# Kernel tuning notes

Hardware: AMD Instinct MI355X
Metric: run time of the kernel (lower is better)

Reference implementation:

```python
import jax, jax.numpy as jnp
import numpy as np

ND, NC = 100000, 20000
E_DD, E_DC, E_CD = 1600000, 800000, 800000
DDIM, CDIM, H, B = 256, 512, 128, 100000


def _lin_init(k, out_d, in_d):
    kw, kb = jax.random.split(k)
    s = 1.0 / np.sqrt(in_d)
    return (jax.random.uniform(kw, (out_d, in_d), jnp.float32, -s, s),
            jax.random.uniform(kb, (out_d,), jnp.float32, -s, s))


def setup_inputs() -> dict:
    key = jax.random.key(0)
    ks = jax.random.split(key, 32)
    inp = {
        'x_drug': jax.random.normal(ks[0], (ND, DDIM), jnp.float32),
        'x_cell': jax.random.normal(ks[1], (NC, CDIM), jnp.float32),
        'ei_dd_src': jax.random.randint(ks[2], (E_DD,), 0, ND),
        'ei_dd_dst': jax.random.randint(ks[3], (E_DD,), 0, ND),
        'ei_dc_src': jax.random.randint(ks[4], (E_DC,), 0, ND),
        'ei_dc_dst': jax.random.randint(ks[5], (E_DC,), 0, NC),
        'ei_cd_src': jax.random.randint(ks[6], (E_CD,), 0, NC),
        'ei_cd_dst': jax.random.randint(ks[7], (E_CD,), 0, ND),
        'q_da': jax.random.randint(ks[8], (B,), 0, ND),
        'q_db': jax.random.randint(ks[9], (B,), 0, ND),
        'q_c': jax.random.randint(ks[10], (B,), 0, NC),
    }
    # input projections
    inp['wd'], inp['bd'] = _lin_init(ks[11], H, DDIM)
    inp['wc'], inp['bc'] = _lin_init(ks[12], H, CDIM)
    # per-edge-type SAGEConv params: lin_l (W+b, on aggregated neighbors), lin_r (W only, on root)
    i = 13
    for name in ['dd1', 'cd1', 'dc1', 'dd2', 'cd2', 'dc2']:
        wl, bl = _lin_init(ks[i], H, H)
        wr, _ = _lin_init(ks[i + 1], H, H)
        inp[name + '_wl'], inp[name + '_bl'], inp[name + '_wr'] = wl, bl, wr
        i += 2
    # MLP head
    inp['m1_w'], inp['m1_b'] = _lin_init(ks[i], H, 3 * H)
    inp['m2_w'], inp['m2_b'] = _lin_init(ks[i + 1], 1, H)
    return inp


def _sage(x_src, x_dst, src, dst, wl, bl, wr):
    # SAGEConv: mean-aggregate neighbor (src) features onto dst, then lin_l + lin_r(root)
    n_dst = x_dst.shape[0]
    agg = jax.ops.segment_sum(x_src[src], dst, num_segments=n_dst)  # [n_dst, H]
    cnt = jax.ops.segment_sum(jnp.ones(src.shape, x_src.dtype), dst, num_segments=n_dst)
    mean = agg / jnp.maximum(cnt, 1.0)[:, None]
    return mean @ wl.T + bl + x_dst @ wr.T


def reference(x_drug, x_cell, wd, bd, wc, bc,
              dd1_wl, dd1_bl, dd1_wr, cd1_wl, cd1_bl, cd1_wr, dc1_wl, dc1_bl, dc1_wr,
              dd2_wl, dd2_bl, dd2_wr, cd2_wl, cd2_bl, cd2_wr, dc2_wl, dc2_bl, dc2_wr,
              m1_w, m1_b, m2_w, m2_b,
              ei_dd_src, ei_dd_dst, ei_dc_src, ei_dc_dst, ei_cd_src, ei_cd_dst,
              q_da, q_db, q_c):
    xd = x_drug @ wd.T + bd  # [ND, H]
    xc = x_cell @ wc.T + bc  # [NC, H]
    # layer 1 (to_hetero: sum contributions per dst node type, then relu)
    hd = jax.nn.relu(_sage(xd, xd, ei_dd_src, ei_dd_dst, dd1_wl, dd1_bl, dd1_wr)
                     + _sage(xc, xd, ei_cd_src, ei_cd_dst, cd1_wl, cd1_bl, cd1_wr))
    hc = jax.nn.relu(_sage(xd, xc, ei_dc_src, ei_dc_dst, dc1_wl, dc1_bl, dc1_wr))
    # layer 2 (no activation)
    od = (_sage(hd, hd, ei_dd_src, ei_dd_dst, dd2_wl, dd2_bl, dd2_wr)
          + _sage(hc, hd, ei_cd_src, ei_cd_dst, cd2_wl, cd2_bl, cd2_wr))
    oc = _sage(hd, hc, ei_dc_src, ei_dc_dst, dc2_wl, dc2_bl, dc2_wr)
    combined = jnp.concatenate([od[q_da], od[q_db], oc[q_c]], axis=-1)  # [B, 3H]
    h = jax.nn.relu(combined @ m1_w.T + m1_b)  # dropout is eval-mode identity
    return (h @ m2_w.T + m2_b)[:, 0]
```

## Files before the change

### kernel.cpp

```cpp
#include <hip/hip_runtime.h>
#include <hip/hip_fp16.h>

typedef _Float16 f16;
typedef f16 f16x8 __attribute__((ext_vector_type(8)));
typedef float f32x4 __attribute__((ext_vector_type(4)));

#define NDRUG 100000
#define NCELL 20000
#define EDD   1600000
#define EDC   800000
#define ECD   800000
#define NQ    100000
#define ETOT  (EDD + ECD + EDC)
#define NNODE 220000

#define NBD 782
#define NBC 313
#define NBTOT (NBD + NBC)
#define ECHUNK 8192
#define NBLK ((ETOT + ECHUNK - 1) / ECHUNK)
#define BCAP 8192
#define LCAP 6144

__device__ inline int bucket_of(int rdst) { return rdst < 200000 ? (rdst >> 8) : NBD + ((rdst - 200000) >> 6); }
__device__ inline int dl_of(int rdst)     { return rdst < 200000 ? (rdst & 255) : ((rdst - 200000) & 63); }


__global__ void initcur_k(int* __restrict__ cur)
{
    int i = blockIdx.x * 256 + threadIdx.x;
    if (i < NBTOT) cur[i] = i * BCAP;
}


__global__ __launch_bounds__(256) void scatter_k(
    const int* __restrict__ dds, const int* __restrict__ ddd,
    const int* __restrict__ cds, const int* __restrict__ cdd,
    const int* __restrict__ dcs, const int* __restrict__ dcd,
    int* __restrict__ bucket_cur, unsigned* __restrict__ binned)
{
    __shared__ int lh[NBTOT];
    __shared__ int lbase[NBTOT];

    int tid = threadIdx.x;
    for (int i = tid; i < NBTOT; i += 256) lh[i] = 0;
    __syncthreads();

    int base = blockIdx.x * ECHUNK;
    int end = base + ECHUNK; if (end > ETOT) end = ETOT;

    for (int e = base + tid; e < end; e += 256) {
        int rdst;
        if (e < EDD) rdst = ddd[e];
        else if (e < EDD + ECD) rdst = 100000 + cdd[e - EDD];
        else rdst = 200000 + dcd[e - EDD - ECD];
        atomicAdd(&lh[bucket_of(rdst)], 1);
    }
    __syncthreads();

    for (int i = tid; i < NBTOT; i += 256) {
        int c = lh[i];
        lbase[i] = c ? atomicAdd(&bucket_cur[i], c) : 0;
        lh[i] = 0;
    }
    __syncthreads();

    for (int e = base + tid; e < end; e += 256) {
        int src, rdst;
        if (e < EDD) { src = dds[e]; rdst = ddd[e]; }
        else if (e < EDD + ECD) { int i2 = e - EDD; src = cds[i2]; rdst = 100000 + cdd[i2]; }
        else { int i2 = e - EDD - ECD; src = dcs[i2]; rdst = 200000 + dcd[i2]; }
        int b = bucket_of(rdst);
        int r = atomicAdd(&lh[b], 1);
        binned[lbase[b] + r] = ((unsigned)dl_of(rdst) << 17) | (unsigned)src;
    }
}


__global__ __launch_bounds__(256) void scan_pbase_k(const int* __restrict__ bucket_cur,
                                                    int* __restrict__ pbase, int* __restrict__ rowptr)
{
    __shared__ int seg[256];
    int tid = threadIdx.x;
    int mine[5], s = 0;
#pragma unroll
    for (int q = 0; q < 5; ++q) {
        int idx = tid * 5 + q;
        int t = 0;
        if (idx < NBTOT) {
            t = bucket_cur[idx] - idx * BCAP;
            t = t < 0 ? 0 : (t > LCAP ? LCAP : t);
        }
        mine[q] = t; s += t;
    }
    seg[tid] = s; __syncthreads();
    for (int o = 1; o < 256; o <<= 1) {
        int v = (tid >= o) ? seg[tid - o] : 0;
        __syncthreads();
        seg[tid] += v;
        __syncthreads();
    }
    int run = seg[tid] - s;
#pragma unroll
    for (int q = 0; q < 5; ++q) {
        int idx = tid * 5 + q;
        if (idx < NBTOT) pbase[idx] = run;
        run += mine[q];
    }
    if (tid == 255) { pbase[NBTOT] = seg[255]; rowptr[NNODE] = seg[255]; }
}


__global__ __launch_bounds__(256) void bucket_build_k(
    const unsigned* __restrict__ binned, const int* __restrict__ bucket_cur, const int* __restrict__ pbase,
    int* __restrict__ rowptr, int* __restrict__ packed)
{
    __shared__ int cnt[256];
    __shared__ int off[256];
    __shared__ int seg[256];
    __shared__ unsigned short lrank[LCAP];
    __shared__ unsigned srec[LCAP];

    int b = blockIdx.x, tid = threadIdx.x;
    int gbase = b * BCAP;
    int n = bucket_cur[b] - gbase;
    n = n < 0 ? 0 : (n > LCAP ? LCAP : n);
    int pb = pbase[b];

    cnt[tid] = 0;
    __syncthreads();
    for (int j = tid; j < n; j += 256) {
        unsigned r = binned[gbase + j];
        lrank[j] = (unsigned short)atomicAdd(&cnt[r >> 17], 1);
    }
    __syncthreads();
    int c = cnt[tid];
    seg[tid] = c; __syncthreads();
    for (int o = 1; o < 256; o <<= 1) {
        int v = (tid >= o) ? seg[tid - o] : 0;
        __syncthreads();
        seg[tid] += v;
        __syncthreads();
    }
    off[tid] = seg[tid] - c;
    __syncthreads();

    if (b < NBD) {
        int rdst = b * 256 + tid;
        if (rdst < 200000) rowptr[rdst] = pb + off[tid];
    } else {
        if (tid < 64) {
            int node = (b - NBD) * 64 + tid;
            if (node < NCELL) rowptr[200000 + node] = pb + off[tid];
        }
    }

    for (int j = tid; j < n; j += 256) {
        unsigned r = binned[gbase + j];
        int p = off[r >> 17] + lrank[j];
        srec[p] = r & 0x1FFFF;
    }
    __syncthreads();

    for (int p = tid; p < n; p += 256) packed[pb + p] = (int)srec[p];
}


__device__ inline void addv(float* acc, uint4 v)
{
    const __half2* h = (const __half2*)&v;
#pragma unroll
    for (int j = 0; j < 4; ++j) {
        float2 f = __half22float2(h[j]);
        acc[2 * j]     += f.x;
        acc[2 * j + 1] += f.y;
    }
}

__global__ __launch_bounds__(256) void agg_all_k(
    const __half* __restrict__ t_d, const __half* __restrict__ t_c,
    const int* __restrict__ rowptr, const int* __restrict__ packed,
    __half* __restrict__ m_a, __half* __restrict__ m_b, __half* __restrict__ m_c)
{
    int gid = blockIdx.x * 16 + (threadIdx.x >> 4);
    if (gid >= NNODE) return;
    int g = threadIdx.x & 15;

    const __half* tab; __half* out;
    if (gid < 100000)      { tab = t_d; out = m_a + (size_t)gid * 128; }
    else if (gid < 200000) { tab = t_c; out = m_b + (size_t)(gid - 100000) * 128; }
    else                   { tab = t_d; out = m_c + (size_t)(gid - 200000) * 128; }

    int s = rowptr[gid];
    int n = rowptr[gid + 1] - s;
    const int* list = packed + s;
    const __half* base = tab + (size_t)g * 8;

    float acc[8];
#pragma unroll
    for (int j = 0; j < 8; ++j) acc[j] = 0.f;

    int i = 0;
    for (; i + 3 < n; i += 4) {
        int s0 = list[i], s1 = list[i + 1], s2 = list[i + 2], s3 = list[i + 3];
        uint4 v0 = *(const uint4*)(base + (size_t)s0 * 128);
        uint4 v1 = *(const uint4*)(base + (size_t)s1 * 128);
        uint4 v2 = *(const uint4*)(base + (size_t)s2 * 128);
        uint4 v3 = *(const uint4*)(base + (size_t)s3 * 128);
        addv(acc, v0); addv(acc, v1); addv(acc, v2); addv(acc, v3);
    }
    for (; i < n; ++i) {
        uint4 v = *(const uint4*)(base + (size_t)list[i] * 128);
        addv(acc, v);
    }

    float inv = 1.f / fmaxf((float)n, 1.f);
    __half h[8];
#pragma unroll
    for (int j = 0; j < 8; ++j) h[j] = __float2half(acc[j] * inv);
    *(uint4*)(out + g * 8) = *(uint4*)h;
}


__global__ __launch_bounds__(256) void prep_k(
    const float* __restrict__ wd,     const float* __restrict__ wc,     const float* __restrict__ m1w,
    const float* __restrict__ dd1_wl, const float* __restrict__ cd1_wl, const float* __restrict__ dc1_wl,
    const float* __restrict__ dc1_wr, const float* __restrict__ dd1_wr, const float* __restrict__ cd1_wr,
    const float* __restrict__ dd1_bl, const float* __restrict__ cd1_bl,
    const float* __restrict__ dd2_wl, const float* __restrict__ cd2_wl, const float* __restrict__ dc2_wl,
    const float* __restrict__ dc2_wr, const float* __restrict__ dd2_wr, const float* __restrict__ cd2_wr,
    const float* __restrict__ dd2_bl, const float* __restrict__ cd2_bl,
    f16* __restrict__ wd16, f16* __restrict__ wc16, f16* __restrict__ m1w16,
    f16* __restrict__ dd1_wl16, f16* __restrict__ cd1_wl16, f16* __restrict__ dc1_wl16,
    f16* __restrict__ dc1_wr16, f16* __restrict__ wr1s16,
    f16* __restrict__ dd2_wl16, f16* __restrict__ cd2_wl16, f16* __restrict__ dc2_wl16,
    f16* __restrict__ dc2_wr16, f16* __restrict__ wr2s16,
    float* __restrict__ bsum1, float* __restrict__ bsum2)
{
    int i = blockIdx.x * 256 + threadIdx.x;
    if (i < 128 * 256) wd16[i] = (f16)wd[i];
    if (i < 128 * 512) wc16[i] = (f16)wc[i];
    if (i < 128 * 384) m1w16[i] = (f16)m1w[i];
    if (i < 128 * 128) {
        dd1_wl16[i] = (f16)dd1_wl[i];
        cd1_wl16[i] = (f16)cd1_wl[i];
        dc1_wl16[i] = (f16)dc1_wl[i];
        dc1_wr16[i] = (f16)dc1_wr[i];
        wr1s16[i]   = (f16)(dd1_wr[i] + cd1_wr[i]);
        dd2_wl16[i] = (f16)dd2_wl[i];
        cd2_wl16[i] = (f16)cd2_wl[i];
        dc2_wl16[i] = (f16)dc2_wl[i];
        dc2_wr16[i] = (f16)dc2_wr[i];
        wr2s16[i]   = (f16)(dd2_wr[i] + cd2_wr[i]);
    }
    if (i < 128) {
        bsum1[i] = dd1_bl[i] + cd1_bl[i];
        bsum2[i] = dd2_bl[i] + cd2_bl[i];
    }
}


template<typename AT, int MODE>
__global__ __launch_bounds__(256) void mgemm_k(
    const AT* A00, const int* I00, const f16* W00, int K00, int S00,
    const AT* A01, const int* I01, const f16* W01, int K01, int S01,
    const AT* A02, const int* I02, const f16* W02, int K02, int S02,
    const float* bias0, f16* Ch0, int M0,
    const AT* A10, const int* I10, const f16* W10, int K10, int S10,
    const AT* A11, const int* I11, const f16* W11, int K11, int S11,
    const AT* A12, const int* I12, const f16* W12, int K12, int S12,
    const float* bias1, f16* Ch1, int M1,
    int split,
    const float* m2w, const float* m2b, float* Cf)
{
    __shared__ f16 As[128][72];
    __shared__ f16 Ws[128][72];

    const int tid = threadIdx.x;
    const int w  = tid >> 6;
    const int l  = tid & 63;
    const int lc = l & 15;
    const int lq = l >> 4;
    const int sr = tid >> 1;
    const int sk = (tid & 1) * 32;

    const bool j1 = (int)blockIdx.x >= split;
    const int mb = ((int)blockIdx.x - (j1 ? split : 0)) * 128;
    const AT*  Aseg[3] = { j1 ? A10 : A00, j1 ? A11 : A01, j1 ? A12 : A02 };
    const int* Iseg[3] = { j1 ? I10 : I00, j1 ? I11 : I01, j1 ? I12 : I02 };
    const f16* Wseg[3] = { j1 ? W10 : W00, j1 ? W11 : W01, j1 ? W12 : W02 };
    const int  Kseg[3] = { j1 ? K10 : K00, j1 ? K11 : K01, j1 ? K12 : K02 };
    const int  Sseg[3] = { j1 ? S10 : S00, j1 ? S11 : S01, j1 ? S12 : S02 };
    const float* bias = j1 ? bias1 : bias0;
    f16* Ch = j1 ? Ch1 : Ch0;
    const int M = j1 ? M1 : M0;

    f32x4 acc[2][8];
#pragma unroll
    for (int mi = 0; mi < 2; ++mi)
#pragma unroll
        for (int j = 0; j < 8; ++j) acc[mi][j] = (f32x4){0.f, 0.f, 0.f, 0.f};

    for (int s = 0; s < 3; ++s) {
        const AT* A = Aseg[s];
        if (!A) continue;
        const int* idx = Iseg[s];
        const f16* W = Wseg[s];
        const int K = Kseg[s], S = Sseg[s];

        int m = mb + sr; if (m >= M) m = M - 1;
        const AT*  arow = A + (size_t)(idx ? idx[m] : m) * (size_t)K;
        const f16* wrow = W + (size_t)sr * (size_t)S;

        for (int kt = 0; kt < K; kt += 64) {
            if constexpr (sizeof(AT) == 2) {
                const uint4* ap = (const uint4*)(arow + kt + sk);
                uint4 a0 = ap[0], a1 = ap[1], a2 = ap[2], a3 = ap[3];
                *(uint4*)&As[sr][sk]      = a0;
                *(uint4*)&As[sr][sk + 8]  = a1;
                *(uint4*)&As[sr][sk + 16] = a2;
                *(uint4*)&As[sr][sk + 24] = a3;
            } else {
                const float4* ap = (const float4*)(arow + kt + sk);
#pragma unroll
                for (int i = 0; i < 4; ++i) {
                    float4 u = ap[2 * i], v = ap[2 * i + 1];
                    f16x8 h;
                    h[0] = (f16)u.x; h[1] = (f16)u.y; h[2] = (f16)u.z; h[3] = (f16)u.w;
                    h[4] = (f16)v.x; h[5] = (f16)v.y; h[6] = (f16)v.z; h[7] = (f16)v.w;
                    *(f16x8*)&As[sr][sk + 8 * i] = h;
                }
            }
            {
                const uint4* wp = (const uint4*)(wrow + kt + sk);
                uint4 w0 = wp[0], w1 = wp[1], w2 = wp[2], w3 = wp[3];
                *(uint4*)&Ws[sr][sk]      = w0;
                *(uint4*)&Ws[sr][sk + 8]  = w1;
                *(uint4*)&Ws[sr][sk + 16] = w2;
                *(uint4*)&Ws[sr][sk + 24] = w3;
            }
            __syncthreads();

#pragma unroll
            for (int ks = 0; ks < 64; ks += 32) {
                f16x8 a0 = *(const f16x8*)&As[32 * w + lc][ks + 8 * lq];
                f16x8 a1 = *(const f16x8*)&As[32 * w + 16 + lc][ks + 8 * lq];
#pragma unroll
                for (int j = 0; j < 8; ++j) {
                    f16x8 b = *(const f16x8*)&Ws[16 * j + lc][ks + 8 * lq];
                    acc[0][j] = __builtin_amdgcn_mfma_f32_16x16x32_f16(a0, b, acc[0][j], 0, 0, 0);
                    acc[1][j] = __builtin_amdgcn_mfma_f32_16x16x32_f16(a1, b, acc[1][j], 0, 0, 0);
                }
            }
            __syncthreads();
        }
    }

    if (MODE == 2) {
        float part[2][4];
#pragma unroll
        for (int mi = 0; mi < 2; ++mi)
#pragma unroll
            for (int r = 0; r < 4; ++r) part[mi][r] = 0.f;
#pragma unroll
        for (int j = 0; j < 8; ++j) {
            float bj = bias[16 * j + lc];
            float wv = m2w[16 * j + lc];
#pragma unroll
            for (int mi = 0; mi < 2; ++mi)
#pragma unroll
                for (int r = 0; r < 4; ++r) {
                    float v = acc[mi][j][r] + bj;
                    v = v > 0.f ? v : 0.f;
                    part[mi][r] = fmaf(v, wv, part[mi][r]);
                }
        }
#pragma unroll
        for (int mi = 0; mi < 2; ++mi)
#pragma unroll
            for (int r = 0; r < 4; ++r) {
                float p = part[mi][r];
#pragma unroll
                for (int o = 1; o < 16; o <<= 1) p += __shfl_xor(p, o, 16);
                if (lc == 0) {
                    int row = mb + 32 * w + 16 * mi + 4 * lq + r;
                    if (row < M) Cf[row] = p + m2b[0];
                }
            }
    } else {
#pragma unroll
        for (int j = 0; j < 8; ++j) {
            float bj = bias[16 * j + lc];
#pragma unroll
            for (int mi = 0; mi < 2; ++mi)
#pragma unroll
                for (int r = 0; r < 4; ++r) {
                    float v = acc[mi][j][r] + bj;
                    if (MODE == 1) v = v > 0.f ? v : 0.f;
                    int row = mb + 32 * w + 16 * mi + 4 * lq + r;
                    if (row < M) Ch[(size_t)row * 128 + 16 * j + lc] = (f16)v;
                }
        }
    }
}


extern "C" void kernel_launch(void* const* d_in, const int* in_sizes, int n_in,
                              void* d_out, int out_size, void* d_ws, size_t ws_size,
                              hipStream_t stream)
{
    const float* x_drug = (const float*)d_in[0];
    const float* x_cell = (const float*)d_in[1];
    const int* ei_dd_src = (const int*)d_in[2];
    const int* ei_dd_dst = (const int*)d_in[3];
    const int* ei_dc_src = (const int*)d_in[4];
    const int* ei_dc_dst = (const int*)d_in[5];
    const int* ei_cd_src = (const int*)d_in[6];
    const int* ei_cd_dst = (const int*)d_in[7];
    const int* q_da = (const int*)d_in[8];
    const int* q_db = (const int*)d_in[9];
    const int* q_c  = (const int*)d_in[10];
    const float* wd = (const float*)d_in[11];
    const float* bd = (const float*)d_in[12];
    const float* wc = (const float*)d_in[13];
    const float* bc = (const float*)d_in[14];
    const float* dd1_wl = (const float*)d_in[15]; const float* dd1_bl = (const float*)d_in[16]; const float* dd1_wr = (const float*)d_in[17];
    const float* cd1_wl = (const float*)d_in[18]; const float* cd1_bl = (const float*)d_in[19]; const float* cd1_wr = (const float*)d_in[20];
    const float* dc1_wl = (const float*)d_in[21]; const float* dc1_bl = (const float*)d_in[22]; const float* dc1_wr = (const float*)d_in[23];
    const float* dd2_wl = (const float*)d_in[24]; const float* dd2_bl = (const float*)d_in[25]; const float* dd2_wr = (const float*)d_in[26];
    const float* cd2_wl = (const float*)d_in[27]; const float* cd2_bl = (const float*)d_in[28]; const float* cd2_wr = (const float*)d_in[29];
    const float* dc2_wl = (const float*)d_in[30]; const float* dc2_bl = (const float*)d_in[31]; const float* dc2_wr = (const float*)d_in[32];
    const float* m1_w = (const float*)d_in[33]; const float* m1_b = (const float*)d_in[34];
    const float* m2_w = (const float*)d_in[35]; const float* m2_b = (const float*)d_in[36];
    float* out = (float*)d_out;

    char* wsp = (char*)d_ws;
    size_t off = 0;
    auto alloc = [&](size_t bytes) -> void* {
        void* p = wsp + off;
        off += (bytes + 255) & ~(size_t)255;
        return p;
    };

    __half* xd_h     = (__half*)alloc((size_t)NDRUG * 128 * 2);
    __half* xc_h     = (__half*)alloc((size_t)NCELL * 128 * 2);
    __half* hd_h     = (__half*)alloc((size_t)NDRUG * 128 * 2);
    __half* hc_h     = (__half*)alloc((size_t)NCELL * 128 * 2);
    __half* mean_a_h = (__half*)alloc((size_t)NDRUG * 128 * 2);
    __half* mean_b_h = (__half*)alloc((size_t)NDRUG * 128 * 2);
    __half* mean_c_h = (__half*)alloc((size_t)NCELL * 128 * 2);
    __half* od_h     = (__half*)alloc((size_t)NDRUG * 128 * 2);
    __half* oc_h     = (__half*)alloc((size_t)NCELL * 128 * 2);

    f16* wd16     = (f16*)alloc(128 * 256 * 2);
    f16* wc16     = (f16*)alloc(128 * 512 * 2);
    f16* m1w16    = (f16*)alloc(128 * 384 * 2);
    f16* dd1_wl16 = (f16*)alloc(128 * 128 * 2);
    f16* cd1_wl16 = (f16*)alloc(128 * 128 * 2);
    f16* dc1_wl16 = (f16*)alloc(128 * 128 * 2);
    f16* dc1_wr16 = (f16*)alloc(128 * 128 * 2);
    f16* wr1s16   = (f16*)alloc(128 * 128 * 2);
    f16* dd2_wl16 = (f16*)alloc(128 * 128 * 2);
    f16* cd2_wl16 = (f16*)alloc(128 * 128 * 2);
    f16* dc2_wl16 = (f16*)alloc(128 * 128 * 2);
    f16* dc2_wr16 = (f16*)alloc(128 * 128 * 2);
    f16* wr2s16   = (f16*)alloc(128 * 128 * 2);
    float* bsum1  = (float*)alloc(128 * 4);
    float* bsum2  = (float*)alloc(128 * 4);

    int* bucket_cur  = (int*)alloc((size_t)NBTOT * 4);
    int* pbase       = (int*)alloc((size_t)(NBTOT + 1) * 4);
    int* rowptr      = (int*)alloc((size_t)(NNODE + 1) * 4);
    int* packed      = (int*)alloc((size_t)ETOT * 4);
    unsigned* binned = (unsigned*)alloc((size_t)NBTOT * BCAP * 4);

    initcur_k<<<(NBTOT + 255) / 256, 256, 0, stream>>>(bucket_cur);
    scatter_k<<<NBLK, 256, 0, stream>>>(ei_dd_src, ei_dd_dst, ei_cd_src, ei_cd_dst,
                                        ei_dc_src, ei_dc_dst, bucket_cur, binned);
    scan_pbase_k<<<1, 256, 0, stream>>>(bucket_cur, pbase, rowptr);
    bucket_build_k<<<NBTOT, 256, 0, stream>>>(binned, bucket_cur, pbase, rowptr, packed);

    prep_k<<<256, 256, 0, stream>>>(
        wd, wc, m1_w,
        dd1_wl, cd1_wl, dc1_wl, dc1_wr, dd1_wr, cd1_wr, dd1_bl, cd1_bl,
        dd2_wl, cd2_wl, dc2_wl, dc2_wr, dd2_wr, cd2_wr, dd2_bl, cd2_bl,
        wd16, wc16, m1w16,
        dd1_wl16, cd1_wl16, dc1_wl16, dc1_wr16, wr1s16,
        dd2_wl16, cd2_wl16, dc2_wl16, dc2_wr16, wr2s16,
        bsum1, bsum2);

    const f16*   fnull = nullptr;
    const float* f32null = nullptr;
    const int*   inull = nullptr;
    const int GD = (NDRUG + 127) / 128;
    const int GC = (NCELL + 127) / 128;
    const int GQ = (NQ + 127) / 128;

    mgemm_k<float, 0><<<GD + GC, 256, 0, stream>>>(
        x_drug, inull, wd16, 256, 256,
        f32null, inull, fnull, 0, 0,
        f32null, inull, fnull, 0, 0,
        bd, (f16*)xd_h, NDRUG,
        x_cell, inull, wc16, 512, 512,
        f32null, inull, fnull, 0, 0,
        f32null, inull, fnull, 0, 0,
        bc, (f16*)xc_h, NCELL,
        GD, f32null, f32null, nullptr);

    const int AGG_GRID = (NNODE + 15) / 16;

    agg_all_k<<<AGG_GRID, 256, 0, stream>>>(xd_h, xc_h, rowptr, packed,
                                            mean_a_h, mean_b_h, mean_c_h);

    mgemm_k<f16, 1><<<GD + GC, 256, 0, stream>>>(
        (const f16*)mean_a_h, inull, dd1_wl16, 128, 128,
        (const f16*)mean_b_h, inull, cd1_wl16, 128, 128,
        (const f16*)xd_h,     inull, wr1s16,   128, 128,
        bsum1, (f16*)hd_h, NDRUG,
        (const f16*)mean_c_h, inull, dc1_wl16, 128, 128,
        (const f16*)xc_h,     inull, dc1_wr16, 128, 128,
        fnull,                inull, fnull,    0, 0,
        dc1_bl, (f16*)hc_h, NCELL,
        GD, f32null, f32null, nullptr);

    agg_all_k<<<AGG_GRID, 256, 0, stream>>>(hd_h, hc_h, rowptr, packed,
                                            mean_a_h, mean_b_h, mean_c_h);

    mgemm_k<f16, 0><<<GD + GC, 256, 0, stream>>>(
        (const f16*)mean_a_h, inull, dd2_wl16, 128, 128,
        (const f16*)mean_b_h, inull, cd2_wl16, 128, 128,
        (const f16*)hd_h,     inull, wr2s16,   128, 128,
        bsum2, (f16*)od_h, NDRUG,
        (const f16*)mean_c_h, inull, dc2_wl16, 128, 128,
        (const f16*)hc_h,     inull, dc2_wr16, 128, 128,
        fnull,                inull, fnull,    0, 0,
        dc2_bl, (f16*)oc_h, NCELL,
        GD, f32null, f32null, nullptr);

    mgemm_k<f16, 2><<<GQ, 256, 0, stream>>>(
        (const f16*)od_h, q_da, m1w16,       128, 384,
        (const f16*)od_h, q_db, m1w16 + 128, 128, 384,
        (const f16*)oc_h, q_c,  m1w16 + 256, 128, 384,
        m1_b, nullptr, NQ,
        fnull, inull, fnull, 0, 0,
        fnull, inull, fnull, 0, 0,
        fnull, inull, fnull, 0, 0,
        f32null, nullptr, 0,
        GQ, m2_w, m2_b, out);
}
```

Measured before the change: 493.2 us.

## Pre-convert input features to fp16, fold cursor init, reorder GEMM segments

Adds a grid-stride kernel that converts x_drug and x_cell from fp32 to fp16, so the input projection GEMM runs on fp16 A operands instead of converting fp32 tiles inline. The bucket-cursor initialisation moves into prep_k, which removes one launch. The cell segments are placed first in the multi-segment GEMMs so the longer-K cell blocks are scheduled early. The cost is an extra read and write pass over about 71 MB of input.

```diff
diff --git a/kernel.cpp b/kernel.cpp
--- a/kernel.cpp
+++ b/kernel.cpp
@@ -26,13 +26,6 @@
 __device__ inline int dl_of(int rdst)     { return rdst < 200000 ? (rdst & 255) : ((rdst - 200000) & 63); }
 
 
-__global__ void initcur_k(int* __restrict__ cur)
-{
-    int i = blockIdx.x * 256 + threadIdx.x;
-    if (i < NBTOT) cur[i] = i * BCAP;
-}
-
-
 __global__ __launch_bounds__(256) void scatter_k(
     const int* __restrict__ dds, const int* __restrict__ ddd,
     const int* __restrict__ cds, const int* __restrict__ cdd,
@@ -163,6 +156,27 @@
     __syncthreads();
 
     for (int p = tid; p < n; p += 256) packed[pb + p] = (int)srec[p];
+}
+
+
+__global__ __launch_bounds__(256) void cvt16_k(const float* __restrict__ xd, f16* __restrict__ xd16,
+                                               const float* __restrict__ xc, f16* __restrict__ xc16)
+{
+    const long TD = (long)NDRUG * 256 / 8;
+    const long TC = (long)NCELL * 512 / 8;
+    long stride = (long)gridDim.x * 256;
+    for (long t = (long)blockIdx.x * 256 + threadIdx.x; t < TD + TC; t += stride) {
+        const float* src; f16* dst;
+        long p;
+        if (t < TD) { src = xd; dst = xd16; p = t; }
+        else        { src = xc; dst = xc16; p = t - TD; }
+        const float4* sp = (const float4*)(src + p * 8);
+        float4 u = sp[0], v = sp[1];
+        f16x8 h;
+        h[0] = (f16)u.x; h[1] = (f16)u.y; h[2] = (f16)u.z; h[3] = (f16)u.w;
+        h[4] = (f16)v.x; h[5] = (f16)v.y; h[6] = (f16)v.z; h[7] = (f16)v.w;
+        *(f16x8*)(dst + p * 8) = h;
+    }
 }
 
 
@@ -235,7 +249,8 @@
     f16* __restrict__ dc1_wr16, f16* __restrict__ wr1s16,
     f16* __restrict__ dd2_wl16, f16* __restrict__ cd2_wl16, f16* __restrict__ dc2_wl16,
     f16* __restrict__ dc2_wr16, f16* __restrict__ wr2s16,
-    float* __restrict__ bsum1, float* __restrict__ bsum2)
+    float* __restrict__ bsum1, float* __restrict__ bsum2,
+    int* __restrict__ bucket_cur)
 {
     int i = blockIdx.x * 256 + threadIdx.x;
     if (i < 128 * 256) wd16[i] = (f16)wd[i];
@@ -257,6 +272,7 @@
         bsum1[i] = dd1_bl[i] + cd1_bl[i];
         bsum2[i] = dd2_bl[i] + cd2_bl[i];
     }
+    if (i < NBTOT) bucket_cur[i] = i * BCAP;
 }
 
 
@@ -442,6 +458,9 @@
         return p;
     };
 
+    f16* xd32_16 = (f16*)alloc((size_t)NDRUG * 256 * 2);
+    f16* xc32_16 = (f16*)alloc((size_t)NCELL * 512 * 2);
+
     __half* xd_h     = (__half*)alloc((size_t)NDRUG * 128 * 2);
     __half* xc_h     = (__half*)alloc((size_t)NCELL * 128 * 2);
     __half* hd_h     = (__half*)alloc((size_t)NDRUG * 128 * 2);
@@ -474,12 +493,6 @@
     int* packed      = (int*)alloc((size_t)ETOT * 4);
     unsigned* binned = (unsigned*)alloc((size_t)NBTOT * BCAP * 4);
 
-    initcur_k<<<(NBTOT + 255) / 256, 256, 0, stream>>>(bucket_cur);
-    scatter_k<<<NBLK, 256, 0, stream>>>(ei_dd_src, ei_dd_dst, ei_cd_src, ei_cd_dst,
-                                        ei_dc_src, ei_dc_dst, bucket_cur, binned);
-    scan_pbase_k<<<1, 256, 0, stream>>>(bucket_cur, pbase, rowptr);
-    bucket_build_k<<<NBTOT, 256, 0, stream>>>(binned, bucket_cur, pbase, rowptr, packed);
-
     prep_k<<<256, 256, 0, stream>>>(
         wd, wc, m1_w,
         dd1_wl, cd1_wl, dc1_wl, dc1_wr, dd1_wr, cd1_wr, dd1_bl, cd1_bl,
@@ -487,7 +500,14 @@
         wd16, wc16, m1w16,
         dd1_wl16, cd1_wl16, dc1_wl16, dc1_wr16, wr1s16,
         dd2_wl16, cd2_wl16, dc2_wl16, dc2_wr16, wr2s16,
-        bsum1, bsum2);
+        bsum1, bsum2, bucket_cur);
+
+    cvt16_k<<<4096, 256, 0, stream>>>(x_drug, xd32_16, x_cell, xc32_16);
+
+    scatter_k<<<NBLK, 256, 0, stream>>>(ei_dd_src, ei_dd_dst, ei_cd_src, ei_cd_dst,
+                                        ei_dc_src, ei_dc_dst, bucket_cur, binned);
+    scan_pbase_k<<<1, 256, 0, stream>>>(bucket_cur, pbase, rowptr);
+    bucket_build_k<<<NBTOT, 256, 0, stream>>>(binned, bucket_cur, pbase, rowptr, packed);
 
     const f16*   fnull = nullptr;
     const float* f32null = nullptr;
@@ -496,16 +516,16 @@
     const int GC = (NCELL + 127) / 128;
     const int GQ = (NQ + 127) / 128;
 
-    mgemm_k<float, 0><<<GD + GC, 256, 0, stream>>>(
-        x_drug, inull, wd16, 256, 256,
-        f32null, inull, fnull, 0, 0,
-        f32null, inull, fnull, 0, 0,
+    mgemm_k<f16, 0><<<GD + GC, 256, 0, stream>>>(
+        xc32_16, inull, wc16, 512, 512,
+        fnull, inull, fnull, 0, 0,
+        fnull, inull, fnull, 0, 0,
+        bc, (f16*)xc_h, NCELL,
+        xd32_16, inull, wd16, 256, 256,
+        fnull, inull, fnull, 0, 0,
+        fnull, inull, fnull, 0, 0,
         bd, (f16*)xd_h, NDRUG,
-        x_cell, inull, wc16, 512, 512,
-        f32null, inull, fnull, 0, 0,
-        f32null, inull, fnull, 0, 0,
-        bc, (f16*)xc_h, NCELL,
-        GD, f32null, f32null, nullptr);
+        GC, f32null, f32null, nullptr);
 
     const int AGG_GRID = (NNODE + 15) / 16;
 
@@ -513,29 +533,29 @@
                                             mean_a_h, mean_b_h, mean_c_h);
 
     mgemm_k<f16, 1><<<GD + GC, 256, 0, stream>>>(
+        (const f16*)mean_c_h, inull, dc1_wl16, 128, 128,
+        (const f16*)xc_h,     inull, dc1_wr16, 128, 128,
+        fnull,                inull, fnull,    0, 0,
+        dc1_bl, (f16*)hc_h, NCELL,
         (const f16*)mean_a_h, inull, dd1_wl16, 128, 128,
         (const f16*)mean_b_h, inull, cd1_wl16, 128, 128,
         (const f16*)xd_h,     inull, wr1s16,   128, 128,
         bsum1, (f16*)hd_h, NDRUG,
-        (const f16*)mean_c_h, inull, dc1_wl16, 128, 128,
-        (const f16*)xc_h,     inull, dc1_wr16, 128, 128,
-        fnull,                inull, fnull,    0, 0,
-        dc1_bl, (f16*)hc_h, NCELL,
-        GD, f32null, f32null, nullptr);
+        GC, f32null, f32null, nullptr);
 
     agg_all_k<<<AGG_GRID, 256, 0, stream>>>(hd_h, hc_h, rowptr, packed,
                                             mean_a_h, mean_b_h, mean_c_h);
 
     mgemm_k<f16, 0><<<GD + GC, 256, 0, stream>>>(
+        (const f16*)mean_c_h, inull, dc2_wl16, 128, 128,
+        (const f16*)hc_h,     inull, dc2_wr16, 128, 128,
+        fnull,                inull, fnull,    0, 0,
+        dc2_bl, (f16*)oc_h, NCELL,
         (const f16*)mean_a_h, inull, dd2_wl16, 128, 128,
         (const f16*)mean_b_h, inull, cd2_wl16, 128, 128,
         (const f16*)hd_h,     inull, wr2s16,   128, 128,
         bsum2, (f16*)od_h, NDRUG,
-        (const f16*)mean_c_h, inull, dc2_wl16, 128, 128,
-        (const f16*)hc_h,     inull, dc2_wr16, 128, 128,
-        fnull,                inull, fnull,    0, 0,
-        dc2_bl, (f16*)oc_h, NCELL,
-        GD, f32null, f32null, nullptr);
+        GC, f32null, f32null, nullptr);
 
     mgemm_k<f16, 2><<<GQ, 256, 0, stream>>>(
         (const f16*)od_h, q_da, m1w16,       128, 384,
```

New measurement: 482.2 us. 1.02x faster.
